# Kernel optimization log

Hardware: AMD Instinct MI355X
Metric: run time of the kernel (lower is better)

Reference implementation:

```python
import jax, jax.numpy as jnp
import numpy as np

# Model dims (match init_kwargs)
B, N, COORD, F0 = 16, 512, 3, 64
K = 8            # kernels per layer
F1, F2 = 128, 256  # conv filters
POOL = 2
FC = 512
EPS = 1e-9


def _pairwise(C):
    """Pairwise euclidean distances D [B,N,N] and direction cosines Cos [B,N,N] from coords C [B,N,3]."""
    dot = jnp.einsum('bic,bjc->bij', C, C)
    l2 = jnp.einsum('bic,bic->bi', C, C)
    d2 = l2[:, :, None] + l2[:, None, :] - 2.0 * dot
    D = jnp.sqrt(jnp.abs(d2) + EPS)
    nrm = jnp.sqrt(l2 + EPS)
    Cos = dot / (nrm[:, :, None] * nrm[:, None, :])
    return D, Cos


def _layer(V, D, Cos, gkw, gkb, acw, acb, gcw, gcb, bng, bnb):
    """GraphKernels -> AngularContribution -> GraphConv -> tanh -> batchnorm (eval)."""
    b, n, f = V.shape
    # GraphKernels: node-dependent learned Gaussian decay over pairwise distances
    u = jax.nn.softplus(V @ gkw + gkb)                # [B,N,K]
    uk = jnp.transpose(u, (0, 2, 1))[..., None]       # [B,K,N,1]
    A = jnp.exp(-(D[:, None] ** 2) * uk)              # [B,K,N,N]
    # AngularContribution: learned interpolation between isotropic and cosine-weighted kernel
    w = jax.nn.sigmoid(V @ acw + acb)                 # [B,N,K]
    wk = jnp.transpose(w, (0, 2, 1))[..., None]       # [B,K,N,1]
    A = A * (wk * Cos[:, None] + (1.0 - wk))          # [B,K,N,N]
    # GraphConv: per-kernel message passing then shared dense over [self || messages]
    M = jnp.einsum('bkij,bjf->bikf', A, V).reshape(b, n, -1)  # [B,N,K*F]
    H = jnp.concatenate([V, M], axis=-1) @ gcw + gcb           # [B,N,F_out]
    H = jnp.tanh(H)
    # batchnorm in eval mode (moving mean 0, var 1): affine only
    return bng * H + bnb


def _pool(V, C, p):
    """AverageSeqGraphPool: average consecutive (sequence-ordered) nodes with window/stride p."""
    b, n, f = V.shape
    return V.reshape(b, n // p, p, f).mean(2), C.reshape(b, n // p, p, -1).mean(2)


def setup_inputs() -> dict:
    key = jax.random.key(0)
    ks = jax.random.split(key, 12)
    def w(k, shape):
        return jax.random.normal(k, shape, jnp.float32) / np.sqrt(shape[0])
    flat_dim = (N // POOL // POOL) * F2
    return {
        'V': jax.random.normal(ks[0], (B, N, F0), jnp.float32),
        'C': jax.random.normal(ks[1], (B, N, COORD), jnp.float32) * 10.0,  # ~Angstrom-scale coords
        'gk_w0': w(ks[2], (F0, K)), 'gk_b0': jnp.zeros((K,), jnp.float32),
        'ac_w0': w(ks[3], (F0, K)), 'ac_b0': jnp.zeros((K,), jnp.float32),
        'gc_w0': w(ks[4], ((K + 1) * F0, F1)), 'gc_b0': jnp.zeros((F1,), jnp.float32),
        'bn_g0': jnp.ones((F1,), jnp.float32), 'bn_b0': jnp.zeros((F1,), jnp.float32),
        'gk_w1': w(ks[5], (F1, K)), 'gk_b1': jnp.zeros((K,), jnp.float32),
        'ac_w1': w(ks[6], (F1, K)), 'ac_b1': jnp.zeros((K,), jnp.float32),
        'gc_w1': w(ks[7], ((K + 1) * F1, F2)), 'gc_b1': jnp.zeros((F2,), jnp.float32),
        'bn_g1': jnp.ones((F2,), jnp.float32), 'bn_b1': jnp.zeros((F2,), jnp.float32),
        'fc_w': w(ks[8], (flat_dim, FC)), 'fc_b': jnp.zeros((FC,), jnp.float32),
    }


def reference(V, C, gk_w0, gk_b0, ac_w0, ac_b0, gc_w0, gc_b0, bn_g0, bn_b0,
              gk_w1, gk_b1, ac_w1, ac_b1, gc_w1, gc_b1, bn_g1, bn_b1, fc_w, fc_b):
    D, Cos = _pairwise(C)
    H = _layer(V, D, Cos, gk_w0, gk_b0, ac_w0, ac_b0, gc_w0, gc_b0, bn_g0, bn_b0)
    H, C1 = _pool(H, C, POOL)
    D, Cos = _pairwise(C1)
    H = _layer(H, D, Cos, gk_w1, gk_b1, ac_w1, ac_b1, gc_w1, gc_b1, bn_g1, bn_b1)
    H, _ = _pool(H, C1, POOL)
    Flat = H.reshape(H.shape[0], -1)  # [B, 128*256]
    return jax.nn.sigmoid(Flat @ fc_w + fc_b)  # [B, 512]
```

## Files before the change

kernel.cpp:

```cpp
#include <hip/hip_runtime.h>
#include <math.h>

#define KK 8
#define EPSF 1e-9f

typedef unsigned int   uint32;
typedef unsigned short u16;
typedef __attribute__((ext_vector_type(8))) short bf16x8;
typedef __attribute__((ext_vector_type(4))) float f32x4;

#define MFMA_16x16x32(a, b, c) __builtin_amdgcn_mfma_f32_16x16x32_bf16(a, b, c, 0, 0, 0)

typedef __attribute__((address_space(1))) const unsigned int glob_cu32;
typedef __attribute__((address_space(3))) unsigned int lds_u32;
__device__ __forceinline__ void g2l16(const void* gsrc, void* ldst) {
    __builtin_amdgcn_global_load_lds((glob_cu32*)gsrc, (lds_u32*)ldst, 16, 0, 0);
}

__device__ __forceinline__ int swz(int row, int o) {
    return (row << 6) + (((o) ^ (row & 7)) << 3);
}

__device__ __forceinline__ float softplusf(float x) {
    return x > 0.0f ? x + log1pf(expf(-x)) : log1pf(expf(x));
}
__device__ __forceinline__ float sigmoidf_(float x) {
    return 1.0f / (1.0f + expf(-x));
}
__device__ __forceinline__ u16 f2bf(float f) {
    union { float f; uint32 u; } v; v.f = f;
    uint32 u = v.u;
    return (u16)((u + 0x7FFFu + ((u >> 16) & 1u)) >> 16);
}
__device__ __forceinline__ uint32 pack2(float a, float b) {
    return (uint32)f2bf(a) | ((uint32)f2bf(b) << 16);
}

__global__ __launch_bounds__(256)
void prep_kernel(const float* __restrict__ V, const float* __restrict__ W0,
                 const float* __restrict__ W1, u16* __restrict__ VT0,
                 u16* __restrict__ Wt0, u16* __restrict__ Wt1) {
    __shared__ float s[64][65];
    int blk = blockIdx.x, tid = threadIdx.x;
    if (blk < 128) {
        int b = blk >> 3, rt = blk & 7;
#pragma unroll
        for (int t = 0; t < 16; t++) {
            int idx = t * 256 + tid; int r = idx >> 6, c = idx & 63;
            s[r][c] = V[((size_t)b * 512 + rt * 64 + r) * 64 + c];
        }
        __syncthreads();
#pragma unroll
        for (int t = 0; t < 16; t++) {
            int idx = t * 256 + tid; int f = idx >> 6, j = idx & 63;
            VT0[((size_t)b * 64 + f) * 512 + rt * 64 + j] = f2bf(s[j][f]);
        }
    } else if (blk < 146) {
        int t0 = blk - 128; int rt = t0 >> 1, ct = t0 & 1;
#pragma unroll
        for (int t = 0; t < 16; t++) {
            int idx = t * 256 + tid; int r = idx >> 6, c = idx & 63;
            s[r][c] = W0[((size_t)rt * 64 + r) * 128 + ct * 64 + c];
        }
        __syncthreads();
#pragma unroll
        for (int t = 0; t < 16; t++) {
            int idx = t * 256 + tid; int f = idx >> 6, j = idx & 63;
            Wt0[((size_t)ct * 64 + f) * 576 + rt * 64 + j] = f2bf(s[j][f]);
        }
    } else {
        int t0 = blk - 146; int rt = t0 >> 2, ct = t0 & 3;
#pragma unroll
        for (int t = 0; t < 16; t++) {
            int idx = t * 256 + tid; int r = idx >> 6, c = idx & 63;
            s[r][c] = W1[((size_t)rt * 64 + r) * 256 + ct * 64 + c];
        }
        __syncthreads();
#pragma unroll
        for (int t = 0; t < 16; t++) {
            int idx = t * 256 + tid; int f = idx >> 6, j = idx & 63;
            Wt1[((size_t)ct * 64 + f) * 1152 + rt * 64 + j] = f2bf(s[j][f]);
        }
    }
}

__global__ __launch_bounds__(256)
void layer0_fused(const u16* __restrict__ VT0, const float* __restrict__ C,
                  const float* __restrict__ V,
                  const float* __restrict__ gw, const float* __restrict__ gb,
                  const float* __restrict__ aw, const float* __restrict__ ab,
                  const u16* __restrict__ Wt0, const float* __restrict__ bias,
                  const float* __restrict__ bng, const float* __restrict__ bnb,
                  float* __restrict__ H0p, u16* __restrict__ VT1) {
    int b = blockIdx.x >> 5, tile = blockIdx.x & 31;
    int i0 = tile * 16;
    int tid = threadIdx.x;
    int wv = tid >> 6, lane = tid & 63, quad = lane >> 4, l15 = lane & 15;

    __shared__ __align__(16) u16 s_mem[16384];
    __shared__ __align__(16) u16 s_X[16 * 584];
    __shared__ __align__(16) float s_ci[16][4];
    __shared__ float s_u[16][KK];
    __shared__ float s_w[16][KK];

    u16* s_vT = s_mem;
    u16* s_A  = s_mem + 4096;

    {
        int t = tid & 127;
        int i = t >> 3, k = t & 7;
        const float4* xr = (const float4*)(V + ((size_t)b * 512 + i0 + i) * 64);
        const float* wm = (tid < 128) ? gw : aw;
        float s = 0.f;
#pragma unroll
        for (int f4 = 0; f4 < 16; f4++) {
            float4 x = xr[f4];
            s += x.x * wm[(f4 * 4 + 0) * 8 + k] + x.y * wm[(f4 * 4 + 1) * 8 + k]
               + x.z * wm[(f4 * 4 + 2) * 8 + k] + x.w * wm[(f4 * 4 + 3) * 8 + k];
        }
        if (tid < 128) s_u[i][k] = softplusf(s + gb[k]);
        else           s_w[i][k] = sigmoidf_(s + ab[k]);
    }
    if (tid < 16) {
        const float* cp = C + ((size_t)b * 512 + i0 + tid) * 3;
        float x = cp[0], y = cp[1], z = cp[2];
        s_ci[tid][0] = x; s_ci[tid][1] = y; s_ci[tid][2] = z;
        s_ci[tid][3] = x * x + y * y + z * z;
    }
    {
        int row = tid >> 4, f4 = tid & 15;
        float4 x = *(const float4*)(V + ((size_t)b * 512 + i0 + row) * 64 + f4 * 4);
        *(uint32*)&s_X[row * 584 + f4 * 4]     = pack2(x.x, x.y);
        *(uint32*)&s_X[row * 584 + f4 * 4 + 2] = pack2(x.z, x.w);
    }

    int ia = tid >> 4, jg = tid & 15;
    int oct = jg >> 1, half = (jg & 1) << 2;

    f32x4 acc[2][4] = {};
    for (int j0 = 0; j0 < 512; j0 += 64) {
        const float4* cp4 = (const float4*)(C + ((size_t)b * 512 + j0 + jg * 4) * 3);
        float4 q0 = cp4[0], q1 = cp4[1], q2 = cp4[2];
        float jx[4] = {q0.x, q0.w, q1.z, q2.y};
        float jy[4] = {q0.y, q1.x, q1.w, q2.z};
        float jz[4] = {q0.z, q1.y, q2.x, q2.w};
        __syncthreads();
#pragma unroll
        for (int p = 0; p < 2; p++) {
            int s = p * 256 + wv * 64 + lane;
            int f = s >> 3, op = s & 7;
            g2l16(VT0 + ((size_t)b * 64 + f) * 512 + j0 + ((op ^ (f & 7)) << 3),
                  (void*)(s_vT + (p * 256 + wv * 64) * 8));
        }
        {
            float cix = s_ci[ia][0], ciy = s_ci[ia][1], ciz = s_ci[ia][2], l2i = s_ci[ia][3];
            float d2a[4], csa[4];
#pragma unroll
            for (int jj = 0; jj < 4; jj++) {
                float l2j = jx[jj] * jx[jj] + jy[jj] * jy[jj] + jz[jj] * jz[jj];
                float dot = cix * jx[jj] + ciy * jy[jj] + ciz * jz[jj];
                d2a[jj] = fabsf(l2i + l2j - 2.f * dot) + EPSF;
                csa[jj] = dot / sqrtf((l2i + EPSF) * (l2j + EPSF));
            }
            const float* up = &s_u[ia][0];
            const float* wp = &s_w[ia][0];
#pragma unroll
            for (int k = 0; k < 8; k++) {
                float uu = up[k], ww = wp[k], om = 1.f - ww;
                float a0 = __expf(-d2a[0] * uu) * (ww * csa[0] + om);
                float a1 = __expf(-d2a[1] * uu) * (ww * csa[1] + om);
                float a2 = __expf(-d2a[2] * uu) * (ww * csa[2] + om);
                float a3 = __expf(-d2a[3] * uu) * (ww * csa[3] + om);
                int row = ia * 8 + k;
                uint2 pk = make_uint2(pack2(a0, a1), pack2(a2, a3));
                *(uint2*)&s_A[(row << 6) + ((oct ^ (row & 7)) << 3) + half] = pk;
            }
        }
        __syncthreads();
#pragma unroll
        for (int ks = 0; ks < 2; ks++) {
            int o = ks * 4 + quad;
            bf16x8 a0 = *(const bf16x8*)&s_A[swz(wv * 32 + l15, o)];
            bf16x8 a1 = *(const bf16x8*)&s_A[swz(wv * 32 + 16 + l15, o)];
#pragma unroll
            for (int cf = 0; cf < 4; cf++) {
                bf16x8 bv = *(const bf16x8*)&s_vT[swz(cf * 16 + l15, o)];
                acc[0][cf] = MFMA_16x16x32(a0, bv, acc[0][cf]);
                acc[1][cf] = MFMA_16x16x32(a1, bv, acc[1][cf]);
            }
        }
    }

#pragma unroll
    for (int rf = 0; rf < 2; rf++)
#pragma unroll
        for (int cf = 0; cf < 4; cf++)
#pragma unroll
            for (int r = 0; r < 4; r++) {
                int arow = wv * 32 + rf * 16 + quad * 4 + r;
                int i = arow >> 3, k = arow & 7;
                s_X[i * 584 + 64 + k * 64 + cf * 16 + l15] = f2bf(acc[rf][cf][r]);
            }
    __syncthreads();

    {
#pragma unroll
        for (int p = 0; p < 4; p++) {
            int s = p * 256 + wv * 64 + lane;
            int cc = s >> 3, op = s & 7;
            g2l16(Wt0 + (size_t)cc * 576 + ((op ^ (cc & 7)) << 3),
                  (void*)(s_mem + (p * 256 + wv * 64) * 8));
        }
    }
    f32x4 acc2[2] = {};
    for (int c = 0; c < 9; c++) {
        u16* cur = s_mem + (c & 1) * 8192;
        u16* nxt = s_mem + ((c + 1) & 1) * 8192;
        __syncthreads();
        if (c < 8) {
            int kcn = (c + 1) * 64;
#pragma unroll
            for (int p = 0; p < 4; p++) {
                int s = p * 256 + wv * 64 + lane;
                int cc = s >> 3, op = s & 7;
                g2l16(Wt0 + (size_t)cc * 576 + kcn + ((op ^ (cc & 7)) << 3),
                      (void*)(nxt + (p * 256 + wv * 64) * 8));
            }
        }
        int kc = c * 64;
#pragma unroll
        for (int ks = 0; ks < 2; ks++) {
            int o = ks * 4 + quad;
            bf16x8 av = *(const bf16x8*)&s_X[l15 * 584 + kc + o * 8];
#pragma unroll
            for (int cf = 0; cf < 2; cf++) {
                bf16x8 bv = *(const bf16x8*)&cur[swz(wv * 32 + cf * 16 + l15, o)];
                acc2[cf] = MFMA_16x16x32(av, bv, acc2[cf]);
            }
        }
    }

#pragma unroll
    for (int cf = 0; cf < 2; cf++) {
        int col = wv * 32 + cf * 16 + l15;
        float bs = bias[col], gg = bng[col], bb = bnb[col];
        float h0 = gg * tanhf(acc2[cf][0] + bs) + bb;
        float h1 = gg * tanhf(acc2[cf][1] + bs) + bb;
        float h2 = gg * tanhf(acc2[cf][2] + bs) + bb;
        float h3 = gg * tanhf(acc2[cf][3] + bs) + bb;
        float p0 = 0.5f * (h0 + h1), p1 = 0.5f * (h2 + h3);
        int pl = tile * 8 + quad * 2;
        H0p[((size_t)b * 256 + pl) * 128 + col] = p0;
        H0p[((size_t)b * 256 + pl + 1) * 128 + col] = p1;
        VT1[((size_t)b * 128 + col) * 256 + pl]     = f2bf(p0);
        VT1[((size_t)b * 128 + col) * 256 + pl + 1] = f2bf(p1);
    }
}

__global__ __launch_bounds__(256)
void layer1_fused(const u16* __restrict__ VT1, const float* __restrict__ C,
                  const float* __restrict__ H0p,
                  const float* __restrict__ gw, const float* __restrict__ gb,
                  const float* __restrict__ aw, const float* __restrict__ ab,
                  const u16* __restrict__ Wt1, const float* __restrict__ bias,
                  const float* __restrict__ bng, const float* __restrict__ bnb,
                  float* __restrict__ H1p) {
    int b = blockIdx.x >> 5, tile = blockIdx.x & 31;
    int i0 = tile * 8;
    int tid = threadIdx.x;
    int wv = tid >> 6, lane = tid & 63, quad = lane >> 4, l15 = lane & 15;

    __shared__ __align__(16) u16 s_mem[16384];
    __shared__ __align__(16) u16 s_X1[8 * 1160];
    __shared__ __align__(16) float s_ci[8][4];
    __shared__ float s_u[8][KK];
    __shared__ float s_w[8][KK];

    u16* s_vT = s_mem;
    u16* s_A  = s_mem + 8192;

    if (wv < 2) {
        int t = tid & 63;
        int i = t >> 3, k = t & 7;
        const float4* xr = (const float4*)(H0p + ((size_t)b * 256 + i0 + i) * 128);
        const float* wm = (wv == 0) ? gw : aw;
        float s = 0.f;
#pragma unroll
        for (int f4 = 0; f4 < 32; f4++) {
            float4 x = xr[f4];
            s += x.x * wm[(f4 * 4 + 0) * 8 + k] + x.y * wm[(f4 * 4 + 1) * 8 + k]
               + x.z * wm[(f4 * 4 + 2) * 8 + k] + x.w * wm[(f4 * 4 + 3) * 8 + k];
        }
        if (wv == 0) s_u[i][k] = softplusf(s + gb[k]);
        else         s_w[i][k] = sigmoidf_(s + ab[k]);
    }
    if (tid < 8) {
        const float* cp = C + ((size_t)b * 512 + 2 * (i0 + tid)) * 3;
        float x = 0.5f * (cp[0] + cp[3]);
        float y = 0.5f * (cp[1] + cp[4]);
        float z = 0.5f * (cp[2] + cp[5]);
        s_ci[tid][0] = x; s_ci[tid][1] = y; s_ci[tid][2] = z;
        s_ci[tid][3] = x * x + y * y + z * z;
    }
    {
        int row = tid >> 5, f4 = tid & 31;
        float4 x = *(const float4*)(H0p + ((size_t)b * 256 + i0 + row) * 128 + f4 * 4);
        *(uint32*)&s_X1[row * 1160 + f4 * 4]     = pack2(x.x, x.y);
        *(uint32*)&s_X1[row * 1160 + f4 * 4 + 2] = pack2(x.z, x.w);
    }

    int kh = tid >> 7, ia = (tid >> 4) & 7, jg = tid & 15;
    int oct = jg >> 1, half = (jg & 1) << 2;

    f32x4 acc[8] = {};
    for (int j0 = 0; j0 < 256; j0 += 64) {
        const float4* cp4 = (const float4*)(C + ((size_t)b * 512 + 2 * (j0 + jg * 4)) * 3);
        float4 q0 = cp4[0], q1 = cp4[1], q2 = cp4[2], q3 = cp4[3], q4 = cp4[4], q5 = cp4[5];
        float r[24] = {q0.x,q0.y,q0.z,q0.w, q1.x,q1.y,q1.z,q1.w, q2.x,q2.y,q2.z,q2.w,
                       q3.x,q3.y,q3.z,q3.w, q4.x,q4.y,q4.z,q4.w, q5.x,q5.y,q5.z,q5.w};
        float jx[4], jy[4], jz[4];
#pragma unroll
        for (int jj = 0; jj < 4; jj++) {
            jx[jj] = 0.5f * (r[6 * jj] + r[6 * jj + 3]);
            jy[jj] = 0.5f * (r[6 * jj + 1] + r[6 * jj + 4]);
            jz[jj] = 0.5f * (r[6 * jj + 2] + r[6 * jj + 5]);
        }
        __syncthreads();
#pragma unroll
        for (int p = 0; p < 4; p++) {
            int s = p * 256 + wv * 64 + lane;
            int f = s >> 3, op = s & 7;
            g2l16(VT1 + ((size_t)b * 128 + f) * 256 + j0 + ((op ^ (f & 7)) << 3),
                  (void*)(s_vT + (p * 256 + wv * 64) * 8));
        }
        {
            float cix = s_ci[ia][0], ciy = s_ci[ia][1], ciz = s_ci[ia][2], l2i = s_ci[ia][3];
            float d2a[4], csa[4];
#pragma unroll
            for (int jj = 0; jj < 4; jj++) {
                float l2j = jx[jj] * jx[jj] + jy[jj] * jy[jj] + jz[jj] * jz[jj];
                float dot = cix * jx[jj] + ciy * jy[jj] + ciz * jz[jj];
                d2a[jj] = fabsf(l2i + l2j - 2.f * dot) + EPSF;
                csa[jj] = dot / sqrtf((l2i + EPSF) * (l2j + EPSF));
            }
            const float* up = &s_u[ia][kh * 4];
            const float* wp = &s_w[ia][kh * 4];
#pragma unroll
            for (int kk = 0; kk < 4; kk++) {
                float uu = up[kk], ww = wp[kk], om = 1.f - ww;
                float a0 = __expf(-d2a[0] * uu) * (ww * csa[0] + om);
                float a1 = __expf(-d2a[1] * uu) * (ww * csa[1] + om);
                float a2 = __expf(-d2a[2] * uu) * (ww * csa[2] + om);
                float a3 = __expf(-d2a[3] * uu) * (ww * csa[3] + om);
                int row = ia * 8 + kh * 4 + kk;
                uint2 pk = make_uint2(pack2(a0, a1), pack2(a2, a3));
                *(uint2*)&s_A[(row << 6) + ((oct ^ (row & 7)) << 3) + half] = pk;
            }
        }
        __syncthreads();
#pragma unroll
        for (int ks = 0; ks < 2; ks++) {
            int o = ks * 4 + quad;
            bf16x8 a0 = *(const bf16x8*)&s_A[swz(wv * 16 + l15, o)];
#pragma unroll
            for (int cf = 0; cf < 8; cf++) {
                bf16x8 bv = *(const bf16x8*)&s_vT[swz(cf * 16 + l15, o)];
                acc[cf] = MFMA_16x16x32(a0, bv, acc[cf]);
            }
        }
    }

#pragma unroll
    for (int cf = 0; cf < 8; cf++)
#pragma unroll
        for (int r = 0; r < 4; r++) {
            int arow = wv * 16 + quad * 4 + r;
            int i = arow >> 3, k = arow & 7;
            s_X1[i * 1160 + 128 + k * 128 + cf * 16 + l15] = f2bf(acc[cf][r]);
        }
    __syncthreads();

    {
#pragma unroll
        for (int p = 0; p < 4; p++) {
            int s = p * 256 + wv * 64 + lane;
            int cc = s >> 3, op = s & 7;
            g2l16(Wt1 + (size_t)cc * 1152 + ((op ^ (cc & 7)) << 3),
                  (void*)(s_mem + (p * 256 + wv * 64) * 8));
        }
    }
    f32x4 acc2[4] = {};
    int g = 0;
    for (int ch = 0; ch < 2; ch++) {
        for (int c = 0; c < 18; c++, g++) {
            u16* cur = s_mem + (g & 1) * 8192;
            u16* nxt = s_mem + ((g + 1) & 1) * 8192;
            __syncthreads();
            if (g < 35) {
                int gn = g + 1;
                int chn = (gn >= 18) ? 1 : 0;
                int colb = chn * 128;
                int kcn = (gn - chn * 18) * 64;
#pragma unroll
                for (int p = 0; p < 4; p++) {
                    int s = p * 256 + wv * 64 + lane;
                    int cc = s >> 3, op = s & 7;
                    g2l16(Wt1 + (size_t)(colb + cc) * 1152 + kcn + ((op ^ (cc & 7)) << 3),
                          (void*)(nxt + (p * 256 + wv * 64) * 8));
                }
            }
            int kc = c * 64;
#pragma unroll
            for (int ks = 0; ks < 2; ks++) {
                int o = ks * 4 + quad;
                bf16x8 av = *(const bf16x8*)&s_X1[(l15 & 7) * 1160 + kc + o * 8];
#pragma unroll
                for (int cf = 0; cf < 2; cf++) {
                    bf16x8 bv = *(const bf16x8*)&cur[swz(wv * 32 + cf * 16 + l15, o)];
                    acc2[ch * 2 + cf] = MFMA_16x16x32(av, bv, acc2[ch * 2 + cf]);
                }
            }
        }
    }

#pragma unroll
    for (int q = 0; q < 4; q++) {
        int ch = q >> 1, cf = q & 1;
        int col = ch * 128 + wv * 32 + cf * 16 + l15;
        float bs = bias[col], gg = bng[col], bb = bnb[col];
        float h0 = gg * tanhf(acc2[q][0] + bs) + bb;
        float h1 = gg * tanhf(acc2[q][1] + bs) + bb;
        float h2 = gg * tanhf(acc2[q][2] + bs) + bb;
        float h3 = gg * tanhf(acc2[q][3] + bs) + bb;
        if (quad < 2) {
            float p0 = 0.5f * (h0 + h1), p1 = 0.5f * (h2 + h3);
            int pl = tile * 4 + quad * 2;
            H1p[((size_t)b * 128 + pl) * 256 + col] = p0;
            H1p[((size_t)b * 128 + pl + 1) * 256 + col] = p1;
        }
    }
}

__global__ __launch_bounds__(256)
void fc_partial_kernel(const float* __restrict__ Flat, const float* __restrict__ W,
                       float* __restrict__ P) {
    int cs = blockIdx.x & 3, ks = blockIdx.x >> 2;
    int m0 = ks * 256;
    int c4 = threadIdx.x & 31;
    int msub = threadIdx.x >> 5;

    __shared__ __align__(16) float xT[256][16];

#pragma unroll
    for (int q = 0; q < 16; q++) {
        int idx = q * 256 + threadIdx.x;
        int b = idx >> 8, mm = idx & 255;
        int bg = (b >> 2) ^ (mm & 3);
        xT[mm][(bg << 2) + (b & 3)] = Flat[(size_t)b * 32768 + m0 + mm];
    }
    __syncthreads();

    const float4* W4 = (const float4*)W;
    float4 acc[16] = {};

    for (int h = 0; h < 4; h++) {
        float4 wbuf[8];
#pragma unroll
        for (int i = 0; i < 8; i++) {
            int mm = msub * 32 + h * 8 + i;
            wbuf[i] = W4[(size_t)(m0 + mm) * 128 + cs * 32 + c4];
        }
#pragma unroll
        for (int i = 0; i < 8; i++) {
            int mm = msub * 32 + h * 8 + i;
#pragma unroll
            for (int bg = 0; bg < 4; bg++) {
                float4 xv = *(const float4*)&xT[mm][((bg ^ (mm & 3)) << 2)];
                acc[bg * 4 + 0].x += xv.x * wbuf[i].x; acc[bg * 4 + 0].y += xv.x * wbuf[i].y;
                acc[bg * 4 + 0].z += xv.x * wbuf[i].z; acc[bg * 4 + 0].w += xv.x * wbuf[i].w;
                acc[bg * 4 + 1].x += xv.y * wbuf[i].x; acc[bg * 4 + 1].y += xv.y * wbuf[i].y;
                acc[bg * 4 + 1].z += xv.y * wbuf[i].z; acc[bg * 4 + 1].w += xv.y * wbuf[i].w;
                acc[bg * 4 + 2].x += xv.z * wbuf[i].x; acc[bg * 4 + 2].y += xv.z * wbuf[i].y;
                acc[bg * 4 + 2].z += xv.z * wbuf[i].z; acc[bg * 4 + 2].w += xv.z * wbuf[i].w;
                acc[bg * 4 + 3].x += xv.w * wbuf[i].x; acc[bg * 4 + 3].y += xv.w * wbuf[i].y;
                acc[bg * 4 + 3].z += xv.w * wbuf[i].z; acc[bg * 4 + 3].w += xv.w * wbuf[i].w;
            }
        }
    }
    __syncthreads();
    __shared__ __align__(16) float red[8][32][4];
#pragma unroll
    for (int b = 0; b < 16; b++) {
        red[msub][c4][0] = acc[b].x; red[msub][c4][1] = acc[b].y;
        red[msub][c4][2] = acc[b].z; red[msub][c4][3] = acc[b].w;
        __syncthreads();
        if (msub == 0) {
            float4 s = make_float4(0.f, 0.f, 0.f, 0.f);
#pragma unroll
            for (int m = 0; m < 8; m++) {
                s.x += red[m][c4][0]; s.y += red[m][c4][1];
                s.z += red[m][c4][2]; s.w += red[m][c4][3];
            }
            *(float4*)&P[((size_t)ks * 16 + b) * 512 + cs * 128 + c4 * 4] = s;
        }
        __syncthreads();
    }
}

__global__ __launch_bounds__(256)
void fc_reduce_kernel(const float* __restrict__ P, const float* __restrict__ fcb,
                      float* __restrict__ out) {
    __shared__ float red[8][33];
    int o = blockIdx.x * 32 + (threadIdx.x & 31);
    int kg = threadIdx.x >> 5;
    float s = 0.f;
#pragma unroll
    for (int q = 0; q < 16; q++) s += P[(size_t)(kg * 16 + q) * 8192 + o];
    red[kg][threadIdx.x & 31] = s;
    __syncthreads();
    if (kg == 0) {
        float t = fcb[o & 511];
#pragma unroll
        for (int m = 0; m < 8; m++) t += red[m][threadIdx.x & 31];
        out[o] = 1.f / (1.f + expf(-t));
    }
}

extern "C" void kernel_launch(void* const* d_in, const int* in_sizes, int n_in,
                              void* d_out, int out_size, void* d_ws, size_t ws_size,
                              hipStream_t stream) {
    const float* V     = (const float*)d_in[0];
    const float* C     = (const float*)d_in[1];
    const float* gk_w0 = (const float*)d_in[2];
    const float* gk_b0 = (const float*)d_in[3];
    const float* ac_w0 = (const float*)d_in[4];
    const float* ac_b0 = (const float*)d_in[5];
    const float* gc_w0 = (const float*)d_in[6];
    const float* gc_b0 = (const float*)d_in[7];
    const float* bn_g0 = (const float*)d_in[8];
    const float* bn_b0 = (const float*)d_in[9];
    const float* gk_w1 = (const float*)d_in[10];
    const float* gk_b1 = (const float*)d_in[11];
    const float* ac_w1 = (const float*)d_in[12];
    const float* ac_b1 = (const float*)d_in[13];
    const float* gc_w1 = (const float*)d_in[14];
    const float* gc_b1 = (const float*)d_in[15];
    const float* bn_g1 = (const float*)d_in[16];
    const float* bn_b1 = (const float*)d_in[17];
    const float* fc_w  = (const float*)d_in[18];
    const float* fc_b  = (const float*)d_in[19];
    float* out = (float*)d_out;

    float* H0p = (float*)d_ws;
    float* H1p = H0p + 524288;
    float* P   = H1p + 524288;
    u16* VT0 = (u16*)(P + 1048576);
    u16* VT1 = VT0 + 524288;
    u16* Wt0 = VT1 + 524288;
    u16* Wt1 = Wt0 + 73728;

    prep_kernel<<<218, 256, 0, stream>>>(V, gc_w0, gc_w1, VT0, Wt0, Wt1);
    layer0_fused<<<512, 256, 0, stream>>>(VT0, C, V, gk_w0, gk_b0, ac_w0, ac_b0,
                                          Wt0, gc_b0, bn_g0, bn_b0, H0p, VT1);
    layer1_fused<<<512, 256, 0, stream>>>(VT1, C, H0p, gk_w1, gk_b1, ac_w1, ac_b1,
                                          Wt1, gc_b1, bn_g1, bn_b1, H1p);
    fc_partial_kernel<<<512, 256, 0, stream>>>(H1p, fc_w, P);
    fc_reduce_kernel<<<256, 256, 0, stream>>>(P, fc_b, out);
}
```

Baseline: 206.4 us.

## Double-buffer V tiles and A generation in the message-passing loops

Both fused layer kernels now keep two shared-memory buffers, each holding a V^T tile and a generated A tile. While the MFMA reduction consumes the current buffer, the DMA for the next V^T tile and the exp/cos A generation for the next tile are issued. This cuts each iteration from two barriers to one and lets the ALU-heavy A generation overlap the matrix-core work. In exchange, shared memory per block grows from 32KB to 48KB in s_mem, which may lower occupancy.

```diff
diff --git a/kernel.cpp b/kernel.cpp
--- a/kernel.cpp
+++ b/kernel.cpp
@@ -97,14 +97,11 @@
     int tid = threadIdx.x;
     int wv = tid >> 6, lane = tid & 63, quad = lane >> 4, l15 = lane & 15;
 
-    __shared__ __align__(16) u16 s_mem[16384];
+    __shared__ __align__(16) u16 s_mem[2][12288];
     __shared__ __align__(16) u16 s_X[16 * 584];
     __shared__ __align__(16) float s_ci[16][4];
     __shared__ float s_u[16][KK];
     __shared__ float s_w[16][KK];
-
-    u16* s_vT = s_mem;
-    u16* s_A  = s_mem + 4096;
 
     {
         int t = tid & 127;
@@ -137,54 +134,73 @@
     int ia = tid >> 4, jg = tid & 15;
     int oct = jg >> 1, half = (jg & 1) << 2;
 
-    f32x4 acc[2][4] = {};
-    for (int j0 = 0; j0 < 512; j0 += 64) {
-        const float4* cp4 = (const float4*)(C + ((size_t)b * 512 + j0 + jg * 4) * 3);
-        float4 q0 = cp4[0], q1 = cp4[1], q2 = cp4[2];
+    auto dmaV = [&](int j0, u16* sV) {
+#pragma unroll
+        for (int p = 0; p < 2; p++) {
+            int s = p * 256 + tid;
+            int f = s >> 3, op = s & 7;
+            g2l16(VT0 + ((size_t)b * 64 + f) * 512 + j0 + ((op ^ (f & 7)) << 3),
+                  (void*)(sV + (p * 256 + wv * 64) * 8));
+        }
+    };
+    auto agen = [&](float4 q0, float4 q1, float4 q2, u16* sA) {
         float jx[4] = {q0.x, q0.w, q1.z, q2.y};
         float jy[4] = {q0.y, q1.x, q1.w, q2.z};
         float jz[4] = {q0.z, q1.y, q2.x, q2.w};
-        __syncthreads();
-#pragma unroll
-        for (int p = 0; p < 2; p++) {
-            int s = p * 256 + wv * 64 + lane;
-            int f = s >> 3, op = s & 7;
-            g2l16(VT0 + ((size_t)b * 64 + f) * 512 + j0 + ((op ^ (f & 7)) << 3),
-                  (void*)(s_vT + (p * 256 + wv * 64) * 8));
-        }
-        {
-            float cix = s_ci[ia][0], ciy = s_ci[ia][1], ciz = s_ci[ia][2], l2i = s_ci[ia][3];
-            float d2a[4], csa[4];
-#pragma unroll
-            for (int jj = 0; jj < 4; jj++) {
-                float l2j = jx[jj] * jx[jj] + jy[jj] * jy[jj] + jz[jj] * jz[jj];
-                float dot = cix * jx[jj] + ciy * jy[jj] + ciz * jz[jj];
-                d2a[jj] = fabsf(l2i + l2j - 2.f * dot) + EPSF;
-                csa[jj] = dot / sqrtf((l2i + EPSF) * (l2j + EPSF));
-            }
-            const float* up = &s_u[ia][0];
-            const float* wp = &s_w[ia][0];
-#pragma unroll
-            for (int k = 0; k < 8; k++) {
-                float uu = up[k], ww = wp[k], om = 1.f - ww;
-                float a0 = __expf(-d2a[0] * uu) * (ww * csa[0] + om);
-                float a1 = __expf(-d2a[1] * uu) * (ww * csa[1] + om);
-                float a2 = __expf(-d2a[2] * uu) * (ww * csa[2] + om);
-                float a3 = __expf(-d2a[3] * uu) * (ww * csa[3] + om);
-                int row = ia * 8 + k;
-                uint2 pk = make_uint2(pack2(a0, a1), pack2(a2, a3));
-                *(uint2*)&s_A[(row << 6) + ((oct ^ (row & 7)) << 3) + half] = pk;
-            }
-        }
-        __syncthreads();
+        float cix = s_ci[ia][0], ciy = s_ci[ia][1], ciz = s_ci[ia][2], l2i = s_ci[ia][3];
+        float d2a[4], csa[4];
+#pragma unroll
+        for (int jj = 0; jj < 4; jj++) {
+            float l2j = jx[jj] * jx[jj] + jy[jj] * jy[jj] + jz[jj] * jz[jj];
+            float dot = cix * jx[jj] + ciy * jy[jj] + ciz * jz[jj];
+            d2a[jj] = fabsf(l2i + l2j - 2.f * dot) + EPSF;
+            csa[jj] = dot / sqrtf((l2i + EPSF) * (l2j + EPSF));
+        }
+        const float* up = &s_u[ia][0];
+        const float* wp = &s_w[ia][0];
+#pragma unroll
+        for (int k = 0; k < 8; k++) {
+            float uu = up[k], ww = wp[k], om = 1.f - ww;
+            float a0 = __expf(-d2a[0] * uu) * (ww * csa[0] + om);
+            float a1 = __expf(-d2a[1] * uu) * (ww * csa[1] + om);
+            float a2 = __expf(-d2a[2] * uu) * (ww * csa[2] + om);
+            float a3 = __expf(-d2a[3] * uu) * (ww * csa[3] + om);
+            int row = ia * 8 + k;
+            uint2 pk = make_uint2(pack2(a0, a1), pack2(a2, a3));
+            *(uint2*)&sA[(row << 6) + ((oct ^ (row & 7)) << 3) + half] = pk;
+        }
+    };
+
+    __syncthreads();
+
+    f32x4 acc[2][4] = {};
+    {
+        const float4* cp4 = (const float4*)(C + ((size_t)b * 512 + jg * 4) * 3);
+        float4 q0 = cp4[0], q1 = cp4[1], q2 = cp4[2];
+        dmaV(0, s_mem[0]);
+        agen(q0, q1, q2, s_mem[0] + 4096);
+    }
+    for (int n = 0; n < 8; n++) {
+        float4 q0, q1, q2;
+        if (n < 7) {
+            const float4* cp4 = (const float4*)(C + ((size_t)b * 512 + (n + 1) * 64 + jg * 4) * 3);
+            q0 = cp4[0]; q1 = cp4[1]; q2 = cp4[2];
+        }
+        __syncthreads();
+        if (n < 7) {
+            dmaV((n + 1) * 64, s_mem[(n + 1) & 1]);
+            agen(q0, q1, q2, s_mem[(n + 1) & 1] + 4096);
+        }
+        const u16* sV = s_mem[n & 1];
+        const u16* sA = s_mem[n & 1] + 4096;
 #pragma unroll
         for (int ks = 0; ks < 2; ks++) {
             int o = ks * 4 + quad;
-            bf16x8 a0 = *(const bf16x8*)&s_A[swz(wv * 32 + l15, o)];
-            bf16x8 a1 = *(const bf16x8*)&s_A[swz(wv * 32 + 16 + l15, o)];
+            bf16x8 a0 = *(const bf16x8*)&sA[swz(wv * 32 + l15, o)];
+            bf16x8 a1 = *(const bf16x8*)&sA[swz(wv * 32 + 16 + l15, o)];
 #pragma unroll
             for (int cf = 0; cf < 4; cf++) {
-                bf16x8 bv = *(const bf16x8*)&s_vT[swz(cf * 16 + l15, o)];
+                bf16x8 bv = *(const bf16x8*)&sV[swz(cf * 16 + l15, o)];
                 acc[0][cf] = MFMA_16x16x32(a0, bv, acc[0][cf]);
                 acc[1][cf] = MFMA_16x16x32(a1, bv, acc[1][cf]);
             }
@@ -203,30 +219,22 @@
             }
     __syncthreads();
 
-    {
+    auto dmaW0 = [&](int kc, u16* buf) {
 #pragma unroll
         for (int p = 0; p < 4; p++) {
-            int s = p * 256 + wv * 64 + lane;
+            int s = p * 256 + tid;
             int cc = s >> 3, op = s & 7;
-            g2l16(Wt0 + (size_t)cc * 576 + ((op ^ (cc & 7)) << 3),
-                  (void*)(s_mem + (p * 256 + wv * 64) * 8));
-        }
-    }
+            g2l16(Wt0 + (size_t)cc * 576 + kc + ((op ^ (cc & 7)) << 3),
+                  (void*)(buf + (p * 256 + wv * 64) * 8));
+        }
+    };
+    dmaW0(0, s_mem[0]);
     f32x4 acc2[2] = {};
     for (int c = 0; c < 9; c++) {
-        u16* cur = s_mem + (c & 1) * 8192;
-        u16* nxt = s_mem + ((c + 1) & 1) * 8192;
-        __syncthreads();
-        if (c < 8) {
-            int kcn = (c + 1) * 64;
-#pragma unroll
-            for (int p = 0; p < 4; p++) {
-                int s = p * 256 + wv * 64 + lane;
-                int cc = s >> 3, op = s & 7;
-                g2l16(Wt0 + (size_t)cc * 576 + kcn + ((op ^ (cc & 7)) << 3),
-                      (void*)(nxt + (p * 256 + wv * 64) * 8));
-            }
-        }
+        u16* cur = s_mem[c & 1];
+        u16* nxt = s_mem[(c + 1) & 1];
+        __syncthreads();
+        if (c < 8) dmaW0((c + 1) * 64, nxt);
         int kc = c * 64;
 #pragma unroll
         for (int ks = 0; ks < 2; ks++) {
@@ -270,14 +278,11 @@
     int tid = threadIdx.x;
     int wv = tid >> 6, lane = tid & 63, quad = lane >> 4, l15 = lane & 15;
 
-    __shared__ __align__(16) u16 s_mem[16384];
+    __shared__ __align__(16) u16 s_mem[2][12288];
     __shared__ __align__(16) u16 s_X1[8 * 1160];
     __shared__ __align__(16) float s_ci[8][4];
     __shared__ float s_u[8][KK];
     __shared__ float s_w[8][KK];
-
-    u16* s_vT = s_mem;
-    u16* s_A  = s_mem + 8192;
 
     if (wv < 2) {
         int t = tid & 63;
@@ -312,12 +317,22 @@
     int kh = tid >> 7, ia = (tid >> 4) & 7, jg = tid & 15;
     int oct = jg >> 1, half = (jg & 1) << 2;
 
-    f32x4 acc[8] = {};
-    for (int j0 = 0; j0 < 256; j0 += 64) {
-        const float4* cp4 = (const float4*)(C + ((size_t)b * 512 + 2 * (j0 + jg * 4)) * 3);
-        float4 q0 = cp4[0], q1 = cp4[1], q2 = cp4[2], q3 = cp4[3], q4 = cp4[4], q5 = cp4[5];
-        float r[24] = {q0.x,q0.y,q0.z,q0.w, q1.x,q1.y,q1.z,q1.w, q2.x,q2.y,q2.z,q2.w,
-                       q3.x,q3.y,q3.z,q3.w, q4.x,q4.y,q4.z,q4.w, q5.x,q5.y,q5.z,q5.w};
+    auto dmaV = [&](int j0, u16* sV) {
+#pragma unroll
+        for (int p = 0; p < 4; p++) {
+            int s = p * 256 + tid;
+            int f = s >> 3, op = s & 7;
+            g2l16(VT1 + ((size_t)b * 128 + f) * 256 + j0 + ((op ^ (f & 7)) << 3),
+                  (void*)(sV + (p * 256 + wv * 64) * 8));
+        }
+    };
+    auto agen = [&](const float4* q, u16* sA) {
+        float r[24];
+#pragma unroll
+        for (int z = 0; z < 6; z++) {
+            r[4 * z] = q[z].x; r[4 * z + 1] = q[z].y;
+            r[4 * z + 2] = q[z].z; r[4 * z + 3] = q[z].w;
+        }
         float jx[4], jy[4], jz[4];
 #pragma unroll
         for (int jj = 0; jj < 4; jj++) {
@@ -325,46 +340,62 @@
             jy[jj] = 0.5f * (r[6 * jj + 1] + r[6 * jj + 4]);
             jz[jj] = 0.5f * (r[6 * jj + 2] + r[6 * jj + 5]);
         }
-        __syncthreads();
-#pragma unroll
-        for (int p = 0; p < 4; p++) {
-            int s = p * 256 + wv * 64 + lane;
-            int f = s >> 3, op = s & 7;
-            g2l16(VT1 + ((size_t)b * 128 + f) * 256 + j0 + ((op ^ (f & 7)) << 3),
-                  (void*)(s_vT + (p * 256 + wv * 64) * 8));
-        }
-        {
-            float cix = s_ci[ia][0], ciy = s_ci[ia][1], ciz = s_ci[ia][2], l2i = s_ci[ia][3];
-            float d2a[4], csa[4];
-#pragma unroll
-            for (int jj = 0; jj < 4; jj++) {
-                float l2j = jx[jj] * jx[jj] + jy[jj] * jy[jj] + jz[jj] * jz[jj];
-                float dot = cix * jx[jj] + ciy * jy[jj] + ciz * jz[jj];
-                d2a[jj] = fabsf(l2i + l2j - 2.f * dot) + EPSF;
-                csa[jj] = dot / sqrtf((l2i + EPSF) * (l2j + EPSF));
-            }
-            const float* up = &s_u[ia][kh * 4];
-            const float* wp = &s_w[ia][kh * 4];
-#pragma unroll
-            for (int kk = 0; kk < 4; kk++) {
-                float uu = up[kk], ww = wp[kk], om = 1.f - ww;
-                float a0 = __expf(-d2a[0] * uu) * (ww * csa[0] + om);
-                float a1 = __expf(-d2a[1] * uu) * (ww * csa[1] + om);
-                float a2 = __expf(-d2a[2] * uu) * (ww * csa[2] + om);
-                float a3 = __expf(-d2a[3] * uu) * (ww * csa[3] + om);
-                int row = ia * 8 + kh * 4 + kk;
-                uint2 pk = make_uint2(pack2(a0, a1), pack2(a2, a3));
-                *(uint2*)&s_A[(row << 6) + ((oct ^ (row & 7)) << 3) + half] = pk;
-            }
-        }
-        __syncthreads();
+        float cix = s_ci[ia][0], ciy = s_ci[ia][1], ciz = s_ci[ia][2], l2i = s_ci[ia][3];
+        float d2a[4], csa[4];
+#pragma unroll
+        for (int jj = 0; jj < 4; jj++) {
+            float l2j = jx[jj] * jx[jj] + jy[jj] * jy[jj] + jz[jj] * jz[jj];
+            float dot = cix * jx[jj] + ciy * jy[jj] + ciz * jz[jj];
+            d2a[jj] = fabsf(l2i + l2j - 2.f * dot) + EPSF;
+            csa[jj] = dot / sqrtf((l2i + EPSF) * (l2j + EPSF));
+        }
+        const float* up = &s_u[ia][kh * 4];
+        const float* wp = &s_w[ia][kh * 4];
+#pragma unroll
+        for (int kk = 0; kk < 4; kk++) {
+            float uu = up[kk], ww = wp[kk], om = 1.f - ww;
+            float a0 = __expf(-d2a[0] * uu) * (ww * csa[0] + om);
+            float a1 = __expf(-d2a[1] * uu) * (ww * csa[1] + om);
+            float a2 = __expf(-d2a[2] * uu) * (ww * csa[2] + om);
+            float a3 = __expf(-d2a[3] * uu) * (ww * csa[3] + om);
+            int row = ia * 8 + kh * 4 + kk;
+            uint2 pk = make_uint2(pack2(a0, a1), pack2(a2, a3));
+            *(uint2*)&sA[(row << 6) + ((oct ^ (row & 7)) << 3) + half] = pk;
+        }
+    };
+
+    __syncthreads();
+
+    f32x4 acc[8] = {};
+    {
+        const float4* cp4 = (const float4*)(C + ((size_t)b * 512 + 2 * (jg * 4)) * 3);
+        float4 q[6];
+#pragma unroll
+        for (int z = 0; z < 6; z++) q[z] = cp4[z];
+        dmaV(0, s_mem[0]);
+        agen(q, s_mem[0] + 8192);
+    }
+    for (int n = 0; n < 4; n++) {
+        float4 q[6];
+        if (n < 3) {
+            const float4* cp4 = (const float4*)(C + ((size_t)b * 512 + 2 * ((n + 1) * 64 + jg * 4)) * 3);
+#pragma unroll
+            for (int z = 0; z < 6; z++) q[z] = cp4[z];
+        }
+        __syncthreads();
+        if (n < 3) {
+            dmaV((n + 1) * 64, s_mem[(n + 1) & 1]);
+            agen(q, s_mem[(n + 1) & 1] + 8192);
+        }
+        const u16* sV = s_mem[n & 1];
+        const u16* sA = s_mem[n & 1] + 8192;
 #pragma unroll
         for (int ks = 0; ks < 2; ks++) {
             int o = ks * 4 + quad;
-            bf16x8 a0 = *(const bf16x8*)&s_A[swz(wv * 16 + l15, o)];
+            bf16x8 a0 = *(const bf16x8*)&sA[swz(wv * 16 + l15, o)];
 #pragma unroll
             for (int cf = 0; cf < 8; cf++) {
-                bf16x8 bv = *(const bf16x8*)&s_vT[swz(cf * 16 + l15, o)];
+                bf16x8 bv = *(const bf16x8*)&sV[swz(cf * 16 + l15, o)];
                 acc[cf] = MFMA_16x16x32(a0, bv, acc[cf]);
             }
         }
@@ -380,34 +411,27 @@
         }
     __syncthreads();
 
-    {
+    auto dmaW1 = [&](int colb, int kc, u16* buf) {
 #pragma unroll
         for (int p = 0; p < 4; p++) {
-            int s = p * 256 + wv * 64 + lane;
+            int s = p * 256 + tid;
             int cc = s >> 3, op = s & 7;
-            g2l16(Wt1 + (size_t)cc * 1152 + ((op ^ (cc & 7)) << 3),
-                  (void*)(s_mem + (p * 256 + wv * 64) * 8));
-        }
-    }
+            g2l16(Wt1 + (size_t)(colb + cc) * 1152 + kc + ((op ^ (cc & 7)) << 3),
+                  (void*)(buf + (p * 256 + wv * 64) * 8));
+        }
+    };
+    dmaW1(0, 0, s_mem[0]);
     f32x4 acc2[4] = {};
     int g = 0;
     for (int ch = 0; ch < 2; ch++) {
         for (int c = 0; c < 18; c++, g++) {
-            u16* cur = s_mem + (g & 1) * 8192;
-            u16* nxt = s_mem + ((g + 1) & 1) * 8192;
+            u16* cur = s_mem[g & 1];
+            u16* nxt = s_mem[(g + 1) & 1];
             __syncthreads();
             if (g < 35) {
                 int gn = g + 1;
                 int chn = (gn >= 18) ? 1 : 0;
-                int colb = chn * 128;
-                int kcn = (gn - chn * 18) * 64;
-#pragma unroll
-                for (int p = 0; p < 4; p++) {
-                    int s = p * 256 + wv * 64 + lane;
-                    int cc = s >> 3, op = s & 7;
-                    g2l16(Wt1 + (size_t)(colb + cc) * 1152 + kcn + ((op ^ (cc & 7)) << 3),
-                          (void*)(nxt + (p * 256 + wv * 64) * 8));
-                }
+                dmaW1(chn * 128, (gn - chn * 18) * 64, nxt);
             }
             int kc = c * 64;
 #pragma unroll
```

Result: no change. 205.9 us (-0.2%).
